# Optimization experiments

Measured on AMD Instinct MI355X. Metric: run time of the kernel, lower is better.

The kernel has to match this reference:

```python
import jax, jax.numpy as jnp
import numpy as np

THETA = 10000.0
AXES_DIM = (16, 56, 56)  # sums to head_dim=128
HEADS = 24
HEAD_DIM = 128
EPS = 1e-5


def _pos_embed(ids):
    # ids: (S, n_axes) int -> cos, sin each (S, head_dim//2)
    pos = ids.astype(jnp.float32)
    cos_out, sin_out = [], []
    for i, d in enumerate(AXES_DIM):
        freqs = 1.0 / (THETA ** (jnp.arange(0, d, 2, dtype=jnp.float32) / d))  # (d/2,)
        ang = pos[:, i][:, None] * freqs[None, :]  # (S, d/2)
        cos_out.append(jnp.cos(ang))
        sin_out.append(jnp.sin(ang))
    return jnp.concatenate(cos_out, -1), jnp.concatenate(sin_out, -1)


def _rms_norm(x, w):
    # per-head RMSNorm over last dim (head_dim)
    var = jnp.mean(x * x, axis=-1, keepdims=True)
    return x * jax.lax.rsqrt(var + EPS) * w


def _apply_rope(x, cos, sin):
    # non-neox (interleaved) rotary. x: (B,S,H,D), cos/sin: (S,D/2)
    x1 = x[..., 0::2]
    x2 = x[..., 1::2]
    c = cos[None, :, None, :]
    s = sin[None, :, None, :]
    o1 = x1 * c - x2 * s
    o2 = x2 * c + x1 * s
    return jnp.stack([o1, o2], axis=-1).reshape(x.shape)


def setup_inputs() -> dict:
    key = jax.random.key(0)
    ks = jax.random.split(key, 12)
    B, S_img, S_txt, D = 1, 2048, 512, 3072
    sd = 1.0 / np.sqrt(D)
    return {
        "hidden_states": jax.random.normal(ks[0], (B, S_img, D), jnp.float32),
        "encoder_hidden_states": jax.random.normal(ks[1], (B, S_txt, D), jnp.float32),
        "ids": jax.random.randint(ks[2], (S_txt + S_img, 3), 0, 64, jnp.int32),
        "w_qkv": jax.random.normal(ks[3], (D, 3 * D), jnp.float32) * sd,
        "w_add_qkv": jax.random.normal(ks[4], (D, 3 * D), jnp.float32) * sd,
        "b_add_qkv": jax.random.normal(ks[5], (3 * D,), jnp.float32) * 0.02,
        "w_out": jax.random.normal(ks[6], (D, D), jnp.float32) * sd,
        "b_out": jax.random.normal(ks[7], (D,), jnp.float32) * 0.02,
        "w_add_out": jax.random.normal(ks[8], (D, D), jnp.float32) * sd,
        "b_add_out": jax.random.normal(ks[9], (D,), jnp.float32) * 0.02,
        "norm_q_w": jnp.ones((HEAD_DIM,), jnp.float32),
        "norm_k_w": jnp.ones((HEAD_DIM,), jnp.float32),
        "norm_add_q_w": jnp.ones((HEAD_DIM,), jnp.float32),
        "norm_add_k_w": jnp.ones((HEAD_DIM,), jnp.float32),
    }


def reference(hidden_states, encoder_hidden_states, ids, w_qkv, w_add_qkv,
              b_add_qkv, w_out, b_out, w_add_out, b_add_out,
              norm_q_w, norm_k_w, norm_add_q_w, norm_add_k_w):
    B, S_img, D = hidden_states.shape
    S_txt = encoder_hidden_states.shape[1]
    H, Dh = HEADS, HEAD_DIM

    # fused QKV projections
    qkv = hidden_states @ w_qkv  # (B, S_img, 3D)
    q, k, v = jnp.split(qkv, 3, axis=-1)
    q = _rms_norm(q.reshape(B, S_img, H, Dh), norm_q_w)
    k = _rms_norm(k.reshape(B, S_img, H, Dh), norm_k_w)
    v = v.reshape(B, S_img, H, Dh)

    eqkv = encoder_hidden_states @ w_add_qkv + b_add_qkv
    eq, ek, ev = jnp.split(eqkv, 3, axis=-1)
    eq = _rms_norm(eq.reshape(B, S_txt, H, Dh), norm_add_q_w)
    ek = _rms_norm(ek.reshape(B, S_txt, H, Dh), norm_add_k_w)
    ev = ev.reshape(B, S_txt, H, Dh)

    # joint sequence: text first, then image
    q = jnp.concatenate([eq, q], axis=1)
    k = jnp.concatenate([ek, k], axis=1)
    v = jnp.concatenate([ev, v], axis=1)

    # multi-axis RoPE over joint positions
    cos, sin = _pos_embed(ids)  # (S_txt+S_img, Dh/2)
    q = _apply_rope(q, cos, sin)
    k = _apply_rope(k, cos, sin)

    # scaled dot-product attention (non-causal)
    scale = 1.0 / np.sqrt(Dh)
    scores = jnp.einsum("bqhd,bkhd->bhqk", q, k) * scale
    probs = jax.nn.softmax(scores, axis=-1)
    attn = jnp.einsum("bhqk,bkhd->bqhd", probs, v)
    attn = attn.reshape(B, S_txt + S_img, H * Dh)

    enc_out = attn[:, :S_txt] @ w_add_out + b_add_out
    img_out = attn[:, S_txt:] @ w_out + b_out
    return img_out, enc_out
```

## Files before the change

kernel.cpp:

```cpp
#include <hip/hip_runtime.h>

typedef __attribute__((ext_vector_type(8))) short short8;
typedef __attribute__((ext_vector_type(4))) short short4v;
typedef __attribute__((ext_vector_type(4))) float floatx4;

__device__ __forceinline__ float b2f(short b) {
  union { unsigned u; float f; } v; v.u = ((unsigned)(unsigned short)b) << 16; return v.f;
}
__device__ __forceinline__ short f2b(float f) {
  union { float f; unsigned u; } v; v.f = f;
  return (short)((v.u + 0x7fffu + ((v.u >> 16) & 1u)) >> 16);
}
__device__ __forceinline__ unsigned cvtpk(float lo, float hi) {
  unsigned r;
  asm("v_cvt_pk_bf16_f32 %0, %1, %2" : "=v"(r) : "v"(lo), "v"(hi));
  return r;
}
__device__ __forceinline__ float loadf(const void* p, size_t i, bool f32) {
  return f32 ? ((const float*)p)[i] : b2f(((const short*)p)[i]);
}
__device__ __forceinline__ short8 load8(const void* p, size_t i, bool f32) {
  if (f32) {
    const float* fp = (const float*)p + i;
    float4 a = *(const float4*)fp;
    float4 b = *(const float4*)(fp + 4);
    short8 r;
    r[0] = f2b(a.x); r[1] = f2b(a.y); r[2] = f2b(a.z); r[3] = f2b(a.w);
    r[4] = f2b(b.x); r[5] = f2b(b.y); r[6] = f2b(b.z); r[7] = f2b(b.w);
    return r;
  }
  return *(const short8*)((const short*)p + i);
}

__device__ __forceinline__ void gload16(const short* g, short* l) {
  __builtin_amdgcn_global_load_lds(
      (const __attribute__((address_space(1))) unsigned int*)g,
      (__attribute__((address_space(3))) unsigned int*)l, 16, 0, 0);
}

__global__ void detect_dtype(const unsigned short* __restrict__ w, int* __restrict__ flag) {
  __shared__ int cnt;
  if (threadIdx.x == 0) cnt = 0;
  __syncthreads();
  int bad = 0;
  for (int i = threadIdx.x; i < 4096; i += 256) {
    int e = (w[i] >> 7) & 0xFF;
    if (e >= 0xC8) bad++;
  }
  atomicAdd(&cnt, bad);
  __syncthreads();
  if (threadIdx.x == 0) *flag = (cnt > 64) ? 1 : 0;
}

__global__ __launch_bounds__(256)
void cvt_bf16_2(const void* __restrict__ srcA, long n8A,
                const void* __restrict__ srcB, long n8B,
                short* __restrict__ dst, const int* __restrict__ dflag) {
  const bool f32 = (*dflag != 0);
  const long n8 = n8A + n8B;
  long stride = (long)gridDim.x * 256;
  for (long i = (long)blockIdx.x * 256 + threadIdx.x; i < n8; i += stride) {
    const void* s; long e;
    if (i < n8A) { s = srcA; e = i * 8; } else { s = srcB; e = (i - n8A) * 8; }
    if (f32) {
      const float* fp = (const float*)s + e;
      float4 a = *(const float4*)fp;
      float4 b = *(const float4*)(fp + 4);
      short8 r;
      r[0] = f2b(a.x); r[1] = f2b(a.y); r[2] = f2b(a.z); r[3] = f2b(a.w);
      r[4] = f2b(b.x); r[5] = f2b(b.y); r[6] = f2b(b.z); r[7] = f2b(b.w);
      *(short8*)(dst + i * 8) = r;
    } else {
      *(short8*)(dst + i * 8) = *(const short8*)((const short*)s + e);
    }
  }
}

__global__ __launch_bounds__(256)
void cvt_tw(const void* __restrict__ wq, short* __restrict__ wqd,
            const void* __restrict__ waq, short* __restrict__ waqd,
            const void* __restrict__ wo, short* __restrict__ wod,
            const void* __restrict__ wao, short* __restrict__ waod,
            const int* __restrict__ dflag) {
  __shared__ short st[64][72];
  const bool f32 = (*dflag != 0);
  const int K = 3072;
  int b = blockIdx.x;
  const void* src; short* dst; int N, n0, k0;
  if (b < 13824) {
    src = (b < 6912) ? wq : waq;
    dst = (b < 6912) ? wqd : waqd;
    int rem = b % 6912;
    N = 9216; n0 = (rem % 144) << 6; k0 = (rem / 144) << 6;
  } else {
    b -= 13824;
    src = (b < 2304) ? wo : wao;
    dst = (b < 2304) ? wod : waod;
    int rem = b % 2304;
    N = 3072; n0 = (rem % 48) << 6; k0 = (rem / 48) << 6;
  }
  const int c4 = threadIdx.x & 15;
  const int rq = threadIdx.x >> 4;
#pragma unroll
  for (int r = 0; r < 4; ++r) {
    int k = r * 16 + rq;
    int n = c4 * 4;
    short v0, v1, v2, v3;
    if (f32) {
      const float* sp = (const float*)src + (size_t)(k0 + k) * N + n0 + n;
      float4 f = *(const float4*)sp;
      v0 = f2b(f.x); v1 = f2b(f.y); v2 = f2b(f.z); v3 = f2b(f.w);
    } else {
      const short* sp = (const short*)src + (size_t)(k0 + k) * N + n0 + n;
      short4v s = *(const short4v*)sp;
      v0 = s[0]; v1 = s[1]; v2 = s[2]; v3 = s[3];
    }
    st[n + 0][k] = v0; st[n + 1][k] = v1; st[n + 2][k] = v2; st[n + 3][k] = v3;
  }
  __syncthreads();
  const int n = threadIdx.x >> 2;
  const int kc = (threadIdx.x & 3) << 4;
  short8 a = *(const short8*)(&st[n][kc]);
  short8 bb = *(const short8*)(&st[n][kc + 8]);
  short* dp = dst + (size_t)(n0 + n) * K + k0 + kc;
  *(short8*)(dp) = a;
  *(short8*)(dp + 8) = bb;
}

__global__ __launch_bounds__(256, 2)
void gemm_bt(const void* __restrict__ A, int a_row0,
             const void* __restrict__ B, const void* __restrict__ bias,
             void* __restrict__ C, int c_row0, int N, int K,
             const int* __restrict__ dflag, int aIn, int cOut) {
  __shared__ short As[128 * 32];
  __shared__ short Bs[128 * 32];
  const bool f32 = (*dflag != 0);
  const bool a32 = aIn && f32;
  const bool c32 = cOut && f32;
  const int tid = threadIdx.x;
  const int lane = tid & 63, w = tid >> 6;
  const int wm = w & 1, wn = w >> 1;
  const int qg = lane >> 4, l16 = lane & 15;
  const int m0 = blockIdx.y << 7, n0 = blockIdx.x << 7;

  const int arow = tid >> 2, ak = (tid & 3) << 3;
  const int brow = tid >> 4, bc = (tid & 15) << 3;
  const int rot = tid & 15;

  floatx4 acc[4][4];
#pragma unroll
  for (int i = 0; i < 4; ++i)
#pragma unroll
    for (int j = 0; j < 4; ++j) acc[i][j] = (floatx4){0.f, 0.f, 0.f, 0.f};

  for (int k0 = 0; k0 < K; k0 += 32) {
    __syncthreads();
#pragma unroll
    for (int j = 0; j < 2; ++j) {
      short8 av = load8(A, (size_t)(a_row0 + m0 + j * 64 + arow) * K + (k0 + ak), a32);
      *(short8*)(As + (j * 64 + arow) * 32 + ak) = av;
      int kr = j * 16 + brow;
      short8 bv = load8(B, (size_t)(k0 + kr) * N + (n0 + bc), f32);
      int kq = kr >> 3, kj = kr & 7;
#pragma unroll
      for (int s = 0; s < 8; ++s) {
        int u = (s + rot) & 7;
        int n = bc + u;
        Bs[(n << 5) + ((kq ^ (n & 3)) << 3) + kj] = bv[u];
      }
    }
    __syncthreads();
    short8 a[4];
#pragma unroll
    for (int mi = 0; mi < 4; ++mi)
      a[mi] = *(const short8*)(As + (wm * 64 + mi * 16 + l16) * 32 + qg * 8);
#pragma unroll
    for (int ni = 0; ni < 4; ++ni) {
      int n = wn * 64 + ni * 16 + l16;
      short8 b = *(const short8*)(Bs + (n << 5) + ((qg ^ (n & 3)) << 3));
#pragma unroll
      for (int mi = 0; mi < 4; ++mi)
        acc[mi][ni] = __builtin_amdgcn_mfma_f32_16x16x32_bf16(a[mi], b, acc[mi][ni], 0, 0, 0);
    }
  }
#pragma unroll
  for (int ni = 0; ni < 4; ++ni) {
    int col = n0 + wn * 64 + ni * 16 + l16;
    float bv = bias ? loadf(bias, col, f32) : 0.0f;
#pragma unroll
    for (int mi = 0; mi < 4; ++mi) {
      int row = m0 + wm * 64 + mi * 16 + qg * 4;
#pragma unroll
      for (int r = 0; r < 4; ++r) {
        size_t idx = (size_t)(c_row0 + row + r) * N + col;
        float val = acc[mi][ni][r] + bv;
        if (c32) ((float*)C)[idx] = val;
        else     ((short*)C)[idx] = f2b(val);
      }
    }
  }
}

__global__ __launch_bounds__(256, 2)
void gemm_bf2(const short* __restrict__ A,
              const short* __restrict__ BTa, const void* __restrict__ biasa,
              int a0a, int c0a, int nYa,
              const short* __restrict__ BTb, const void* __restrict__ biasb,
              int a0b, int c0b,
              void* __restrict__ C, int N, int K,
              const int* __restrict__ dflag, int cOut) {
  __shared__ short Ls[3 * 8192 + 3 * 4096];
#define ASB(b) (Ls + (b) * 8192)
#define BSB(b) (Ls + 24576 + (b) * 4096)
  const bool f32 = (*dflag != 0);
  const bool c32 = cOut && f32;
  const int bx = blockIdx.x;
  const int y = blockIdx.y;
  const short* BT; const void* bias; int arow0, crow0;
  if (y < nYa) { BT = BTa; bias = biasa; arow0 = a0a + (y << 8); crow0 = c0a + (y << 8); }
  else { int my = y - nYa; BT = BTb; bias = biasb; arow0 = a0b + (my << 8); crow0 = c0b + (my << 8); }
  const int tid = threadIdx.x;
  const int lane = tid & 63, w = tid >> 6;
  const int wm = w & 1, wn = w >> 1;
  const int qg = lane >> 4, l16 = lane & 15;
  const int n0 = bx << 7;
  const int garow = lane >> 2;
  const int gcir = lane & 3;
  const int nk = K >> 5;
  const int swz = (gcir ^ (garow & 3) ^ (garow >> 2)) << 3;
  const short* Abase = A + (size_t)(arow0 + w * 64 + garow) * K + swz;
  const short* Bbase = BT + (size_t)(n0 + w * 32 + garow) * K + swz;
  const int rswz = (l16 & 3) ^ (l16 >> 2);

  floatx4 acc[8][4];
#pragma unroll
  for (int i = 0; i < 8; ++i)
#pragma unroll
    for (int j = 0; j < 4; ++j) acc[i][j] = (floatx4){0.f, 0.f, 0.f, 0.f};

  auto STAGE = [&](int buf, int k0) {
#pragma unroll
    for (int j = 0; j < 4; ++j)
      gload16(Abase + (size_t)j * 16 * K + k0, ASB(buf) + ((w * 4 + j) << 9));
#pragma unroll
    for (int j = 0; j < 2; ++j)
      gload16(Bbase + (size_t)j * 16 * K + k0, BSB(buf) + ((w * 2 + j) << 9));
  };

  STAGE(0, 0);
  if (nk > 1) STAGE(1, 32);

  int cb = 0;
  for (int t = 0; t < nk; ++t) {
    if (t + 1 < nk) {
      asm volatile("s_waitcnt vmcnt(6) lgkmcnt(0)" ::: "memory");
    } else {
      asm volatile("s_waitcnt vmcnt(0) lgkmcnt(0)" ::: "memory");
    }
    __builtin_amdgcn_s_barrier();
    if (t + 2 < nk) {
      int sb = (cb == 0) ? 2 : cb - 1;
      STAGE(sb, (t + 2) << 5);
    }
    short8 a[8], b[4];
#pragma unroll
    for (int mi = 0; mi < 8; ++mi) {
      int ra = wm * 128 + mi * 16 + l16;
      a[mi] = *(const short8*)(ASB(cb) + (ra << 5) + ((qg ^ rswz) << 3));
    }
#pragma unroll
    for (int ni = 0; ni < 4; ++ni) {
      int n = wn * 64 + ni * 16 + l16;
      b[ni] = *(const short8*)(BSB(cb) + (n << 5) + ((qg ^ rswz) << 3));
    }
    __builtin_amdgcn_s_setprio(1);
#pragma unroll
    for (int ni = 0; ni < 4; ++ni)
#pragma unroll
      for (int mi = 0; mi < 8; ++mi)
        acc[mi][ni] = __builtin_amdgcn_mfma_f32_16x16x32_bf16(a[mi], b[ni], acc[mi][ni], 0, 0, 0);
    __builtin_amdgcn_s_setprio(0);
    cb = (cb == 2) ? 0 : cb + 1;
  }
  __builtin_amdgcn_s_barrier();
  if (!c32) {
    short* wreg = Ls + w * 4096;
#pragma unroll
    for (int half = 0; half < 2; ++half) {
#pragma unroll
      for (int ni = 0; ni < 4; ++ni) {
        float bvv = bias ? loadf(bias, n0 + wn * 64 + ni * 16 + l16, f32) : 0.0f;
#pragma unroll
        for (int mi2 = 0; mi2 < 4; ++mi2)
#pragma unroll
          for (int r = 0; r < 4; ++r)
            wreg[(mi2 * 16 + qg * 4 + r) * 64 + ni * 16 + l16] =
                f2b(acc[half * 4 + mi2][ni][r] + bvv);
      }
      asm volatile("s_waitcnt lgkmcnt(0)" ::: "memory");
#pragma unroll
      for (int j = 0; j < 8; ++j) {
        int row = j * 8 + (lane >> 3);
        int col = (lane & 7) * 8;
        short8 v = *(const short8*)(wreg + row * 64 + col);
        *(short8*)((short*)C + (size_t)(crow0 + wm * 128 + half * 64 + row) * N +
                   n0 + wn * 64 + col) = v;
      }
      asm volatile("s_waitcnt lgkmcnt(0)" ::: "memory");
    }
  } else {
    float* wregf = (float*)(Ls) + w * 2048;
#pragma unroll
    for (int half = 0; half < 2; ++half) {
#pragma unroll
      for (int ch = 0; ch < 2; ++ch) {
#pragma unroll
        for (int nh = 0; nh < 2; ++nh) {
          int ni = ch * 2 + nh;
          float bvv = bias ? loadf(bias, n0 + wn * 64 + ni * 16 + l16, f32) : 0.0f;
#pragma unroll
          for (int mi2 = 0; mi2 < 4; ++mi2)
#pragma unroll
            for (int r = 0; r < 4; ++r)
              wregf[(mi2 * 16 + qg * 4 + r) * 32 + nh * 16 + l16] =
                  acc[half * 4 + mi2][ni][r] + bvv;
        }
        asm volatile("s_waitcnt lgkmcnt(0)" ::: "memory");
#pragma unroll
        for (int j = 0; j < 8; ++j) {
          int row = j * 8 + (lane >> 3);
          int c4 = (lane & 7) * 4;
          float4 v = *(const float4*)(wregf + row * 32 + c4);
          *(float4*)((float*)C + (size_t)(crow0 + wm * 128 + half * 64 + row) * N +
                     n0 + wn * 64 + ch * 32 + c4) = v;
        }
        asm volatile("s_waitcnt lgkmcnt(0)" ::: "memory");
      }
    }
  }
#undef ASB
#undef BSB
}

__global__ __launch_bounds__(256, 3)
void gemm_bf128(const short* __restrict__ A,
                const short* __restrict__ BTa, const void* __restrict__ biasa,
                int a0a, int c0a, int nYa,
                const short* __restrict__ BTb, const void* __restrict__ biasb,
                int a0b, int c0b,
                void* __restrict__ C, int N, int K,
                const int* __restrict__ dflag, int cOut) {
  __shared__ short Ls[6 * 128 * 32];
#define ASB(b) (Ls + (b) * 4096)
#define BSB(b) (Ls + (3 + (b)) * 4096)
  const bool f32 = (*dflag != 0);
  const bool c32 = cOut && f32;
  const int bx = blockIdx.x;
  const int y = blockIdx.y;
  const short* BT; const void* bias; int arow0, crow0;
  if (y < nYa) { BT = BTa; bias = biasa; arow0 = a0a + (y << 7); crow0 = c0a + (y << 7); }
  else { int my = y - nYa; BT = BTb; bias = biasb; arow0 = a0b + (my << 7); crow0 = c0b + (my << 7); }
  const int tid = threadIdx.x;
  const int lane = tid & 63, w = tid >> 6;
  const int wm = w & 1, wn = w >> 1;
  const int qg = lane >> 4, l16 = lane & 15;
  const int n0 = bx << 7;
  const int garow = lane >> 2;
  const int gcir = lane & 3;
  const int nk = K >> 5;
  const int swz = (gcir ^ (garow & 3) ^ (garow >> 2)) << 3;
  const short* Abase = A + (size_t)(arow0 + w * 32 + garow) * K + swz;
  const short* Bbase = BT + (size_t)(n0 + w * 32 + garow) * K + swz;
  const int rswz = (l16 & 3) ^ (l16 >> 2);

  floatx4 acc[4][4];
#pragma unroll
  for (int i = 0; i < 4; ++i)
#pragma unroll
    for (int j = 0; j < 4; ++j) acc[i][j] = (floatx4){0.f, 0.f, 0.f, 0.f};

  auto STAGE = [&](int buf, int k0) {
#pragma unroll
    for (int j = 0; j < 2; ++j) {
      gload16(Abase + (size_t)j * 16 * K + k0, ASB(buf) + ((w * 2 + j) << 9));
      gload16(Bbase + (size_t)j * 16 * K + k0, BSB(buf) + ((w * 2 + j) << 9));
    }
  };

  STAGE(0, 0);
  if (nk > 1) STAGE(1, 32);

  int cb = 0;
  for (int t = 0; t < nk; ++t) {
    if (t + 1 < nk) {
      asm volatile("s_waitcnt vmcnt(4) lgkmcnt(0)" ::: "memory");
    } else {
      asm volatile("s_waitcnt vmcnt(0) lgkmcnt(0)" ::: "memory");
    }
    __builtin_amdgcn_s_barrier();
    if (t + 2 < nk) {
      int sb = (cb == 0) ? 2 : cb - 1;
      STAGE(sb, (t + 2) << 5);
    }
    short8 a[4], b[4];
#pragma unroll
    for (int mi = 0; mi < 4; ++mi) {
      int ra = wm * 64 + mi * 16 + l16;
      a[mi] = *(const short8*)(ASB(cb) + (ra << 5) + ((qg ^ rswz) << 3));
    }
#pragma unroll
    for (int ni = 0; ni < 4; ++ni) {
      int n = wn * 64 + ni * 16 + l16;
      b[ni] = *(const short8*)(BSB(cb) + (n << 5) + ((qg ^ rswz) << 3));
    }
    __builtin_amdgcn_s_setprio(1);
#pragma unroll
    for (int ni = 0; ni < 4; ++ni)
#pragma unroll
      for (int mi = 0; mi < 4; ++mi)
        acc[mi][ni] = __builtin_amdgcn_mfma_f32_16x16x32_bf16(a[mi], b[ni], acc[mi][ni], 0, 0, 0);
    __builtin_amdgcn_s_setprio(0);
    cb = (cb == 2) ? 0 : cb + 1;
  }
  __builtin_amdgcn_s_barrier();
  if (!c32) {
    short* wreg = Ls + w * 4096;
#pragma unroll
    for (int ni = 0; ni < 4; ++ni) {
      float bvv = bias ? loadf(bias, n0 + wn * 64 + ni * 16 + l16, f32) : 0.0f;
#pragma unroll
      for (int mi = 0; mi < 4; ++mi)
#pragma unroll
        for (int r = 0; r < 4; ++r)
          wreg[(mi * 16 + qg * 4 + r) * 64 + ni * 16 + l16] = f2b(acc[mi][ni][r] + bvv);
    }
    asm volatile("s_waitcnt lgkmcnt(0)" ::: "memory");
#pragma unroll
    for (int j = 0; j < 8; ++j) {
      int row = j * 8 + (lane >> 3);
      int col = (lane & 7) * 8;
      short8 v = *(const short8*)(wreg + row * 64 + col);
      *(short8*)((short*)C + (size_t)(crow0 + wm * 64 + row) * N + n0 + wn * 64 + col) = v;
    }
  } else {
    float* wregf = (float*)(Ls) + w * 2048;
#pragma unroll
    for (int half = 0; half < 2; ++half) {
#pragma unroll
      for (int nh = 0; nh < 2; ++nh) {
        int ni = half * 2 + nh;
        float bvv = bias ? loadf(bias, n0 + wn * 64 + ni * 16 + l16, f32) : 0.0f;
#pragma unroll
        for (int mi = 0; mi < 4; ++mi)
#pragma unroll
          for (int r = 0; r < 4; ++r)
            wregf[(mi * 16 + qg * 4 + r) * 32 + nh * 16 + l16] = acc[mi][ni][r] + bvv;
      }
      asm volatile("s_waitcnt lgkmcnt(0)" ::: "memory");
#pragma unroll
      for (int j = 0; j < 8; ++j) {
        int row = j * 8 + (lane >> 3);
        int c4 = (lane & 7) * 4;
        float4 v = *(const float4*)(wregf + row * 32 + c4);
        *(float4*)((float*)C + (size_t)(crow0 + wm * 64 + row) * N + n0 + wn * 64 + half * 32 + c4) = v;
      }
      asm volatile("s_waitcnt lgkmcnt(0)" ::: "memory");
    }
  }
#undef ASB
#undef BSB
}

__global__ __launch_bounds__(512)
void norm_rope(short* __restrict__ qkv, const int* __restrict__ ids,
               const void* __restrict__ nqw, const void* __restrict__ nkw,
               const void* __restrict__ naqw, const void* __restrict__ nakw,
               const int* __restrict__ dflag) {
  const bool f32 = (*dflag != 0);
  const int t = blockIdx.x, wv = threadIdx.x >> 6, lane = threadIdx.x & 63;
  const bool txt = t < 512;
  int p = lane, axis; float expo;
  if (p < 8)       { axis = 0; expo = (float)(2 * p) * (1.0f / 16.0f); }
  else if (p < 36) { axis = 1; expo = (float)(2 * (p - 8)) * (1.0f / 56.0f); }
  else             { axis = 2; expo = (float)(2 * (p - 36)) * (1.0f / 56.0f); }
  float freq = __expf(-expo * 9.210340371976184f);
  float ang = (float)ids[t * 3 + axis] * freq;
  float s, c; sincosf(ang, &s, &c);
  const void* qw = txt ? naqw : nqw;
  const void* kw = txt ? nakw : nkw;
  float w0q = loadf(qw, 2 * lane, f32), w1q = loadf(qw, 2 * lane + 1, f32);
  float w0k = loadf(kw, 2 * lane, f32), w1k = loadf(kw, 2 * lane + 1, f32);
  const float QS = 0.08838834764831845f * 1.4426950408889634f;
#pragma unroll
  for (int i = 0; i < 3; ++i) {
    int h = wv + 8 * i;
    short* qp = qkv + (size_t)t * 9216 + h * 128 + 2 * lane;
    short* kp = qp + 3072;
    union { unsigned u; short sh[2]; } qv, kv;
    qv.u = *(const unsigned*)qp;
    kv.u = *(const unsigned*)kp;
    float q0 = b2f(qv.sh[0]), q1 = b2f(qv.sh[1]);
    float k0 = b2f(kv.sh[0]), k1 = b2f(kv.sh[1]);
    float sq = q0 * q0 + q1 * q1, sk = k0 * k0 + k1 * k1;
#pragma unroll
    for (int o = 1; o < 64; o <<= 1) { sq += __shfl_xor(sq, o); sk += __shfl_xor(sk, o); }
    float rq = rsqrtf(sq * (1.0f / 128.0f) + 1e-5f);
    float rk = rsqrtf(sk * (1.0f / 128.0f) + 1e-5f);
    float qn0 = q0 * rq * w0q, qn1 = q1 * rq * w1q;
    float kn0 = k0 * rk * w0k, kn1 = k1 * rk * w1k;
    float qo0 = qn0 * c - qn1 * s, qo1 = qn1 * c + qn0 * s;
    float ko0 = kn0 * c - kn1 * s, ko1 = kn1 * c + kn0 * s;
    union { unsigned u; short sh[2]; } qo, ko;
    qo.sh[0] = f2b(qo0 * QS);
    qo.sh[1] = f2b(qo1 * QS);
    ko.sh[0] = f2b(ko0); ko.sh[1] = f2b(ko1);
    *(unsigned*)qp = qo.u;
    *(unsigned*)kp = ko.u;
  }
}

__global__ __launch_bounds__(512, 2)
void attn_fa(const short* __restrict__ qkv, short* __restrict__ attn) {
  __shared__ short QPs[256 * 128];
  __shared__ short KVs[2][128 * 128];
  const int wgid = blockIdx.x;
  const int xcd = wgid & 7, slot = wgid >> 3;
  const int h = xcd * 3 + slot / 10;
  const int qt = slot % 10;
  const int tid = threadIdx.x, lane = tid & 63, w = tid >> 6;
  const int qg = lane >> 4, l16 = lane & 15;
  const int lr = lane >> 4, lc = lane & 15;
  const int q0 = qt << 8;
  const int sc = tid & 15;
  const int srow5 = (tid >> 4) & 15, half = tid >> 8;

  const short* Qg  = qkv + (size_t)q0 * 9216 + h * 128;
  const short* Kg0 = qkv + 3072 + h * 128;
  const short* Vg0 = qkv + 6144 + h * 128;

  short8 vr[4];
#pragma unroll
  for (int j = 0; j < 8; ++j) {
    int row = j * 32 + w * 4 + lr;
    gload16(Qg + (size_t)row * 9216 + ((lc ^ (row & 7)) << 3),
            QPs + (j * 32 + w * 4) * 128);
  }
#pragma unroll
  for (int j = 0; j < 4; ++j) {
    int row = j * 32 + w * 4 + lr;
    gload16(Kg0 + (size_t)row * 9216 + ((lc ^ (row & 7)) << 3),
            &KVs[0][(j * 32 + w * 4) * 128]);
  }
#pragma unroll
  for (int j = 0; j < 4; ++j) {
    int row = half * 64 + j * 16 + srow5;
    vr[j] = *(const short8*)(Vg0 + (size_t)row * 9216 + sc * 8);
  }
  asm volatile("s_waitcnt vmcnt(8) lgkmcnt(0)" ::: "memory");
  __builtin_amdgcn_s_barrier();
  short8 aq[2][4];
#pragma unroll
  for (int mi = 0; mi < 2; ++mi)
#pragma unroll
    for (int kc = 0; kc < 4; ++kc) {
      int row = w * 32 + mi * 16 + l16;
      aq[mi][kc] = *(const short8*)(QPs + row * 128 + (((kc * 4 + qg) ^ (row & 7)) << 3));
    }

  floatx4 acc_o[2][8];
#pragma unroll
  for (int mi = 0; mi < 2; ++mi)
#pragma unroll
    for (int nd = 0; nd < 8; ++nd) acc_o[mi][nd] = (floatx4){0.f, 0.f, 0.f, 0.f};
  float m_i[2][4], l_i[2][4];
#pragma unroll
  for (int mi = 0; mi < 2; ++mi)
#pragma unroll
    for (int r = 0; r < 4; ++r) { m_i[mi][r] = -1e30f; l_i[mi][r] = 0.0f; }

  for (int kt = 0; kt < 20; ++kt) {
    const int c = kt & 1;
    asm volatile("s_waitcnt vmcnt(4) lgkmcnt(0)" ::: "memory");
    __builtin_amdgcn_s_barrier();
    if (kt < 19) {
      const short* Kg = qkv + ((size_t)(kt + 1) * 128) * 9216 + 3072 + h * 128;
#pragma unroll
      for (int j = 0; j < 4; ++j) {
        int row = j * 32 + w * 4 + lr;
        gload16(Kg + (size_t)row * 9216 + ((lc ^ (row & 7)) << 3),
                &KVs[1 - c][(j * 32 + w * 4) * 128]);
      }
    }
    floatx4 acc_s[2][8];
#pragma unroll
    for (int mi = 0; mi < 2; ++mi)
#pragma unroll
      for (int ni = 0; ni < 8; ++ni) acc_s[mi][ni] = (floatx4){0.f, 0.f, 0.f, 0.f};
    __builtin_amdgcn_s_setprio(1);
#pragma unroll
    for (int kc = 0; kc < 4; ++kc) {
#pragma unroll
      for (int ni = 0; ni < 8; ++ni) {
        int row = ni * 16 + l16;
        short8 b = *(const short8*)(&KVs[c][row * 128 + (((kc * 4 + qg) ^ (row & 7)) << 3)]);
        acc_s[0][ni] = __builtin_amdgcn_mfma_f32_16x16x32_bf16(aq[0][kc], b, acc_s[0][ni], 0, 0, 0);
        acc_s[1][ni] = __builtin_amdgcn_mfma_f32_16x16x32_bf16(aq[1][kc], b, acc_s[1][ni], 0, 0, 0);
      }
    }
    __builtin_amdgcn_s_setprio(0);
    float mxv[2][4];
    bool need = false;
#pragma unroll
    for (int mi = 0; mi < 2; ++mi) {
#pragma unroll
      for (int r = 0; r < 4; ++r) {
        float mx = acc_s[mi][0][r];
#pragma unroll
        for (int ni = 1; ni < 8; ++ni) mx = fmaxf(mx, acc_s[mi][ni][r]);
        mx = fmaxf(mx, __shfl_xor(mx, 1));
        mx = fmaxf(mx, __shfl_xor(mx, 2));
        mx = fmaxf(mx, __shfl_xor(mx, 4));
        mx = fmaxf(mx, __shfl_xor(mx, 8));
        mxv[mi][r] = mx;
        need = need || (mx > m_i[mi][r] + 8.0f);
      }
    }
    if (__ballot(need)) {
#pragma unroll
      for (int mi = 0; mi < 2; ++mi) {
#pragma unroll
        for (int r = 0; r < 4; ++r) {
          float mn = fmaxf(m_i[mi][r], mxv[mi][r]);
          float al = __builtin_amdgcn_exp2f(m_i[mi][r] - mn);
          m_i[mi][r] = mn;
          l_i[mi][r] *= al;
#pragma unroll
          for (int nd = 0; nd < 8; ++nd) acc_o[mi][nd][r] *= al;
        }
      }
    }
#pragma unroll
    for (int mi = 0; mi < 2; ++mi) {
      float rs[4] = {0.f, 0.f, 0.f, 0.f};
#pragma unroll
      for (int r = 0; r < 4; ++r) {
        float pv[8];
#pragma unroll
        for (int ni = 0; ni < 8; ++ni) {
          pv[ni] = __builtin_amdgcn_exp2f(acc_s[mi][ni][r] - m_i[mi][r]);
          rs[r] += pv[ni];
        }
        unsigned u0 = cvtpk(pv[0], pv[1]);
        unsigned u1 = cvtpk(pv[2], pv[3]);
        unsigned u2 = cvtpk(pv[4], pv[5]);
        unsigned u3 = cvtpk(pv[6], pv[7]);
        int row = w * 32 + mi * 16 + qg * 4 + r;
        uint4 uu; uu.x = u0; uu.y = u1; uu.z = u2; uu.w = u3;
        *(uint4*)(QPs + row * 128 + ((l16 ^ (row & 15)) << 3)) = uu;
      }
#pragma unroll
      for (int r = 0; r < 4; ++r) {
        float t = rs[r];
        t += __shfl_xor(t, 1); t += __shfl_xor(t, 2);
        t += __shfl_xor(t, 4); t += __shfl_xor(t, 8);
        l_i[mi][r] += t;
      }
    }
    asm volatile("s_waitcnt lgkmcnt(0)" ::: "memory");
    __builtin_amdgcn_s_barrier();
#pragma unroll
    for (int u = 0; u < 8; ++u) {
      int d = sc * 8 + u;
      short4v pk = { vr[0][u], vr[1][u], vr[2][u], vr[3][u] };
      *(short4v*)(&KVs[c][d * 128 + (((srow5 ^ u ^ (sc & 7))) << 3) + half * 4]) = pk;
    }
    if (kt < 19) {
      const short* Vg = qkv + ((size_t)(kt + 1) * 128) * 9216 + 6144 + h * 128;
#pragma unroll
      for (int j = 0; j < 4; ++j) {
        int row = half * 64 + j * 16 + srow5;
        vr[j] = *(const short8*)(Vg + (size_t)row * 9216 + sc * 8);
      }
    }
    asm volatile("s_waitcnt lgkmcnt(0)" ::: "memory");
    __builtin_amdgcn_s_barrier();
    __builtin_amdgcn_s_setprio(1);
#pragma unroll
    for (int kc = 0; kc < 4; ++kc) {
      int prow0 = w * 32 + l16;
      short8 ap0 = *(const short8*)(QPs + prow0 * 128 + (((kc * 4 + qg) ^ (prow0 & 15)) << 3));
      int prow1 = prow0 + 16;
      short8 ap1 = *(const short8*)(QPs + prow1 * 128 + (((kc * 4 + qg) ^ (prow1 & 15)) << 3));
#pragma unroll
      for (int nd = 0; nd < 8; ++nd) {
        int row = nd * 16 + l16;
        int chn = (kc * 4 + qg) ^ (row & 7) ^ ((row >> 3) & 7);
        short8 b = *(const short8*)(&KVs[c][row * 128 + (chn << 3)]);
        acc_o[0][nd] = __builtin_amdgcn_mfma_f32_16x16x32_bf16(ap0, b, acc_o[0][nd], 0, 0, 0);
        acc_o[1][nd] = __builtin_amdgcn_mfma_f32_16x16x32_bf16(ap1, b, acc_o[1][nd], 0, 0, 0);
      }
    }
    __builtin_amdgcn_s_setprio(0);
  }
#pragma unroll
  for (int mi = 0; mi < 2; ++mi) {
    float inv[4];
#pragma unroll
    for (int r = 0; r < 4; ++r) inv[r] = 1.0f / l_i[mi][r];
#pragma unroll
    for (int nd = 0; nd < 8; ++nd) {
#pragma unroll
      for (int r = 0; r < 4; ++r) {
        int row = w * 32 + mi * 16 + qg * 4 + r;
        QPs[row * 128 + nd * 16 + l16] = f2b(acc_o[mi][nd][r] * inv[r]);
      }
    }
  }
  asm volatile("s_waitcnt lgkmcnt(0)" ::: "memory");
#pragma unroll
  for (int j = 0; j < 8; ++j) {
    int rrow = w * 32 + j * 4 + qg;
    short8 vv = *(const short8*)(QPs + rrow * 128 + l16 * 8);
    *(short8*)(attn + (size_t)(q0 + rrow) * 3072 + h * 128 + l16 * 8) = vv;
  }
}

extern "C" void kernel_launch(void* const* d_in, const int* in_sizes, int n_in,
                              void* d_out, int out_size, void* d_ws, size_t ws_size,
                              hipStream_t stream) {
  (void)in_sizes; (void)n_in; (void)out_size;
  const void* hidden    = d_in[0];
  const void* enc       = d_in[1];
  const int*  ids       = (const int*)d_in[2];
  const void* w_qkv     = d_in[3];
  const void* w_add_qkv = d_in[4];
  const void* b_add_qkv = d_in[5];
  const void* w_out     = d_in[6];
  const void* b_out     = d_in[7];
  const void* w_add_out = d_in[8];
  const void* b_add_out = d_in[9];
  const void* nqw  = d_in[10];
  const void* nkw  = d_in[11];
  const void* naqw = d_in[12];
  const void* nakw = d_in[13];

  int*   dflag = (int*)d_ws;
  short* qkv   = (short*)((char*)d_ws + 256);
  short* attnB = qkv + (size_t)2560 * 9216;

  short* pool  = attnB + (size_t)2560 * 3072;
  const long n_hid  = 2048L * 3072;
  const long n_enc  = 512L * 3072;
  const long n_wqkv = 3072L * 9216;
  const long n_wout = 3072L * 3072;
  short* xb   = pool;
  short* wqb  = xb + n_enc + n_hid;
  short* waqb = wqb + n_wqkv;
  short* wob  = waqb + n_wqkv;
  short* waob = wob + n_wout;
  const size_t REQ = 256 + 2 * ((size_t)2560 * 9216 + (size_t)2560 * 3072 +
                                n_hid + n_enc + 2 * n_wqkv + 2 * n_wout);

  detect_dtype<<<1, 256, 0, stream>>>((const unsigned short*)w_qkv, dflag);

  if (ws_size >= REQ) {
    cvt_bf16_2<<<1024, 256, 0, stream>>>(enc, n_enc / 8, hidden, n_hid / 8, xb, dflag);
    cvt_tw<<<dim3(18432), 256, 0, stream>>>(w_qkv, wqb, w_add_qkv, waqb,
                                            w_out, wob, w_add_out, waob, dflag);

    gemm_bf2<<<dim3(72, 10), 256, 0, stream>>>(
        xb, waqb, b_add_qkv, 0, 0, 2, wqb, nullptr, 512, 512,
        qkv, 9216, 3072, dflag, 0);
    norm_rope<<<dim3(2560), 512, 0, stream>>>(qkv, ids, nqw, nkw, naqw, nakw, dflag);
    attn_fa<<<dim3(240), 512, 0, stream>>>(qkv, attnB);
    gemm_bf128<<<dim3(24, 20), 256, 0, stream>>>(
        attnB, wob, b_out, 512, 0, 16, waob, b_add_out, 0, 2048,
        d_out, 3072, 3072, dflag, 1);
  } else {
    gemm_bt<<<dim3(72, 4), 256, 0, stream>>>(enc, 0, w_add_qkv, b_add_qkv, qkv, 0, 9216, 3072, dflag, 1, 0);
    gemm_bt<<<dim3(72, 16), 256, 0, stream>>>(hidden, 0, w_qkv, nullptr, qkv, 512, 9216, 3072, dflag, 1, 0);
    norm_rope<<<dim3(2560), 512, 0, stream>>>(qkv, ids, nqw, nkw, naqw, nakw, dflag);
    attn_fa<<<dim3(240), 512, 0, stream>>>(qkv, attnB);
    gemm_bt<<<dim3(24, 16), 256, 0, stream>>>(attnB, 512, w_out, b_out, d_out, 0, 3072, 3072, dflag, 0, 1);
    gemm_bt<<<dim3(24, 4), 256, 0, stream>>>(attnB, 0, w_add_out, b_add_out, d_out, 2048, 3072, 3072, dflag, 0, 1);
  }
}
```

Measured before the change: 792.8 us.

## Halve attention query tile to 128 rows and stage P per-wave

The flash-attention kernel now handles 128 query rows per workgroup instead of 256, so each wave owns 16 rows and the grid doubles from 240 to 480 blocks. Q is loaded straight from global memory into registers rather than through LDS. The P tile passes through a small per-wave LDS buffer per k-chunk instead of a full 256x128 shared tile, and the V transpose layout changes to match. This is meant to spread work across more CUs and cut LDS footprint. The cost is twice the K/V global traffic per query and half the MFMA reuse of each K/V fragment.

```diff
diff --git a/kernel.cpp b/kernel.cpp
--- a/kernel.cpp
+++ b/kernel.cpp
@@ -521,16 +521,16 @@
 
 __global__ __launch_bounds__(512, 2)
 void attn_fa(const short* __restrict__ qkv, short* __restrict__ attn) {
-  __shared__ short QPs[256 * 128];
   __shared__ short KVs[2][128 * 128];
+  __shared__ short Pw[8][512];
   const int wgid = blockIdx.x;
   const int xcd = wgid & 7, slot = wgid >> 3;
-  const int h = xcd * 3 + slot / 10;
-  const int qt = slot % 10;
+  const int h = xcd * 3 + slot / 20;
+  const int qt = slot % 20;
   const int tid = threadIdx.x, lane = tid & 63, w = tid >> 6;
   const int qg = lane >> 4, l16 = lane & 15;
   const int lr = lane >> 4, lc = lane & 15;
-  const int q0 = qt << 8;
+  const int q0 = qt << 7;
   const int sc = tid & 15;
   const int srow5 = (tid >> 4) & 15, half = tid >> 8;
 
@@ -538,19 +538,17 @@
   const short* Kg0 = qkv + 3072 + h * 128;
   const short* Vg0 = qkv + 6144 + h * 128;
 
-  short8 vr[4];
-#pragma unroll
-  for (int j = 0; j < 8; ++j) {
-    int row = j * 32 + w * 4 + lr;
-    gload16(Qg + (size_t)row * 9216 + ((lc ^ (row & 7)) << 3),
-            QPs + (j * 32 + w * 4) * 128);
-  }
 #pragma unroll
   for (int j = 0; j < 4; ++j) {
     int row = j * 32 + w * 4 + lr;
     gload16(Kg0 + (size_t)row * 9216 + ((lc ^ (row & 7)) << 3),
             &KVs[0][(j * 32 + w * 4) * 128]);
   }
+  short8 aq[4];
+#pragma unroll
+  for (int kc = 0; kc < 4; ++kc)
+    aq[kc] = *(const short8*)(Qg + (size_t)(w * 16 + l16) * 9216 + kc * 32 + qg * 8);
+  short8 vr[4];
 #pragma unroll
   for (int j = 0; j < 4; ++j) {
     int row = half * 64 + j * 16 + srow5;
@@ -558,28 +556,16 @@
   }
   asm volatile("s_waitcnt vmcnt(8) lgkmcnt(0)" ::: "memory");
   __builtin_amdgcn_s_barrier();
-  short8 aq[2][4];
-#pragma unroll
-  for (int mi = 0; mi < 2; ++mi)
-#pragma unroll
-    for (int kc = 0; kc < 4; ++kc) {
-      int row = w * 32 + mi * 16 + l16;
-      aq[mi][kc] = *(const short8*)(QPs + row * 128 + (((kc * 4 + qg) ^ (row & 7)) << 3));
-    }
-
-  floatx4 acc_o[2][8];
-#pragma unroll
-  for (int mi = 0; mi < 2; ++mi)
-#pragma unroll
-    for (int nd = 0; nd < 8; ++nd) acc_o[mi][nd] = (floatx4){0.f, 0.f, 0.f, 0.f};
-  float m_i[2][4], l_i[2][4];
-#pragma unroll
-  for (int mi = 0; mi < 2; ++mi)
-#pragma unroll
-    for (int r = 0; r < 4; ++r) { m_i[mi][r] = -1e30f; l_i[mi][r] = 0.0f; }
+
+  floatx4 acc_o[8];
+#pragma unroll
+  for (int nd = 0; nd < 8; ++nd) acc_o[nd] = (floatx4){0.f, 0.f, 0.f, 0.f};
+  float m_i[4], l_i[4];
+#pragma unroll
+  for (int r = 0; r < 4; ++r) { m_i[r] = -1e30f; l_i[r] = 0.0f; }
 
   for (int kt = 0; kt < 20; ++kt) {
-    const int c = kt & 1;
+    const int cb = kt & 1;
     asm volatile("s_waitcnt vmcnt(4) lgkmcnt(0)" ::: "memory");
     __builtin_amdgcn_s_barrier();
     if (kt < 19) {
@@ -588,91 +574,78 @@
       for (int j = 0; j < 4; ++j) {
         int row = j * 32 + w * 4 + lr;
         gload16(Kg + (size_t)row * 9216 + ((lc ^ (row & 7)) << 3),
-                &KVs[1 - c][(j * 32 + w * 4) * 128]);
-      }
-    }
-    floatx4 acc_s[2][8];
-#pragma unroll
-    for (int mi = 0; mi < 2; ++mi)
-#pragma unroll
-      for (int ni = 0; ni < 8; ++ni) acc_s[mi][ni] = (floatx4){0.f, 0.f, 0.f, 0.f};
+                &KVs[1 - cb][(j * 32 + w * 4) * 128]);
+      }
+    }
+    floatx4 acc_s[8];
+#pragma unroll
+    for (int ni = 0; ni < 8; ++ni) acc_s[ni] = (floatx4){0.f, 0.f, 0.f, 0.f};
     __builtin_amdgcn_s_setprio(1);
 #pragma unroll
     for (int kc = 0; kc < 4; ++kc) {
 #pragma unroll
       for (int ni = 0; ni < 8; ++ni) {
         int row = ni * 16 + l16;
-        short8 b = *(const short8*)(&KVs[c][row * 128 + (((kc * 4 + qg) ^ (row & 7)) << 3)]);
-        acc_s[0][ni] = __builtin_amdgcn_mfma_f32_16x16x32_bf16(aq[0][kc], b, acc_s[0][ni], 0, 0, 0);
-        acc_s[1][ni] = __builtin_amdgcn_mfma_f32_16x16x32_bf16(aq[1][kc], b, acc_s[1][ni], 0, 0, 0);
+        short8 b = *(const short8*)(&KVs[cb][row * 128 + (((kc * 4 + qg) ^ (row & 7)) << 3)]);
+        acc_s[ni] = __builtin_amdgcn_mfma_f32_16x16x32_bf16(aq[kc], b, acc_s[ni], 0, 0, 0);
       }
     }
     __builtin_amdgcn_s_setprio(0);
-    float mxv[2][4];
+    float mxv[4];
     bool need = false;
 #pragma unroll
-    for (int mi = 0; mi < 2; ++mi) {
+    for (int r = 0; r < 4; ++r) {
+      float mx = acc_s[0][r];
+#pragma unroll
+      for (int ni = 1; ni < 8; ++ni) mx = fmaxf(mx, acc_s[ni][r]);
+      mx = fmaxf(mx, __shfl_xor(mx, 1));
+      mx = fmaxf(mx, __shfl_xor(mx, 2));
+      mx = fmaxf(mx, __shfl_xor(mx, 4));
+      mx = fmaxf(mx, __shfl_xor(mx, 8));
+      mxv[r] = mx;
+      need = need || (mx > m_i[r] + 8.0f);
+    }
+    if (__ballot(need)) {
 #pragma unroll
       for (int r = 0; r < 4; ++r) {
-        float mx = acc_s[mi][0][r];
-#pragma unroll
-        for (int ni = 1; ni < 8; ++ni) mx = fmaxf(mx, acc_s[mi][ni][r]);
-        mx = fmaxf(mx, __shfl_xor(mx, 1));
-        mx = fmaxf(mx, __shfl_xor(mx, 2));
-        mx = fmaxf(mx, __shfl_xor(mx, 4));
-        mx = fmaxf(mx, __shfl_xor(mx, 8));
-        mxv[mi][r] = mx;
-        need = need || (mx > m_i[mi][r] + 8.0f);
-      }
-    }
-    if (__ballot(need)) {
-#pragma unroll
-      for (int mi = 0; mi < 2; ++mi) {
-#pragma unroll
-        for (int r = 0; r < 4; ++r) {
-          float mn = fmaxf(m_i[mi][r], mxv[mi][r]);
-          float al = __builtin_amdgcn_exp2f(m_i[mi][r] - mn);
-          m_i[mi][r] = mn;
-          l_i[mi][r] *= al;
-#pragma unroll
-          for (int nd = 0; nd < 8; ++nd) acc_o[mi][nd][r] *= al;
-        }
-      }
-    }
-#pragma unroll
-    for (int mi = 0; mi < 2; ++mi) {
-      float rs[4] = {0.f, 0.f, 0.f, 0.f};
-#pragma unroll
-      for (int r = 0; r < 4; ++r) {
-        float pv[8];
-#pragma unroll
-        for (int ni = 0; ni < 8; ++ni) {
-          pv[ni] = __builtin_amdgcn_exp2f(acc_s[mi][ni][r] - m_i[mi][r]);
-          rs[r] += pv[ni];
-        }
-        unsigned u0 = cvtpk(pv[0], pv[1]);
-        unsigned u1 = cvtpk(pv[2], pv[3]);
-        unsigned u2 = cvtpk(pv[4], pv[5]);
-        unsigned u3 = cvtpk(pv[6], pv[7]);
-        int row = w * 32 + mi * 16 + qg * 4 + r;
-        uint4 uu; uu.x = u0; uu.y = u1; uu.z = u2; uu.w = u3;
-        *(uint4*)(QPs + row * 128 + ((l16 ^ (row & 15)) << 3)) = uu;
-      }
-#pragma unroll
-      for (int r = 0; r < 4; ++r) {
-        float t = rs[r];
-        t += __shfl_xor(t, 1); t += __shfl_xor(t, 2);
-        t += __shfl_xor(t, 4); t += __shfl_xor(t, 8);
-        l_i[mi][r] += t;
-      }
+        float mn = fmaxf(m_i[r], mxv[r]);
+        float al = __builtin_amdgcn_exp2f(m_i[r] - mn);
+        m_i[r] = mn;
+        l_i[r] *= al;
+#pragma unroll
+        for (int nd = 0; nd < 8; ++nd) acc_o[nd][r] *= al;
+      }
+    }
+    unsigned pkr[4][4];
+#pragma unroll
+    for (int r = 0; r < 4; ++r) {
+      float pv[8];
+      float rs = 0.f;
+#pragma unroll
+      for (int ni = 0; ni < 8; ++ni) {
+        pv[ni] = __builtin_amdgcn_exp2f(acc_s[ni][r] - m_i[r]);
+        rs += pv[ni];
+      }
+#pragma unroll
+      for (int kc = 0; kc < 4; ++kc) pkr[r][kc] = cvtpk(pv[2 * kc], pv[2 * kc + 1]);
+      rs += __shfl_xor(rs, 1); rs += __shfl_xor(rs, 2);
+      rs += __shfl_xor(rs, 4); rs += __shfl_xor(rs, 8);
+      l_i[r] += rs;
     }
     asm volatile("s_waitcnt lgkmcnt(0)" ::: "memory");
     __builtin_amdgcn_s_barrier();
 #pragma unroll
     for (int u = 0; u < 8; ++u) {
       int d = sc * 8 + u;
-      short4v pk = { vr[0][u], vr[1][u], vr[2][u], vr[3][u] };
-      *(short4v*)(&KVs[c][d * 128 + (((srow5 ^ u ^ (sc & 7))) << 3) + half * 4]) = pk;
+      int xr = (d & 7) ^ ((d >> 3) & 7);
+#pragma unroll
+      for (int jp = 0; jp < 2; ++jp) {
+        int kcw = 2 * half + jp;
+        int g = kcw * 4 + (srow5 >> 2);
+        union { unsigned uu; short sh[2]; } pk;
+        pk.sh[0] = vr[2 * jp][u]; pk.sh[1] = vr[2 * jp + 1][u];
+        *(unsigned*)(&KVs[cb][d * 128 + ((g ^ xr) << 3) + ((2 * srow5) & 7)]) = pk.uu;
+      }
     }
     if (kt < 19) {
       const short* Vg = qkv + ((size_t)(kt + 1) * 128) * 9216 + 6144 + h * 128;
@@ -687,40 +660,38 @@
     __builtin_amdgcn_s_setprio(1);
 #pragma unroll
     for (int kc = 0; kc < 4; ++kc) {
-      int prow0 = w * 32 + l16;
-      short8 ap0 = *(const short8*)(QPs + prow0 * 128 + (((kc * 4 + qg) ^ (prow0 & 15)) << 3));
-      int prow1 = prow0 + 16;
-      short8 ap1 = *(const short8*)(QPs + prow1 * 128 + (((kc * 4 + qg) ^ (prow1 & 15)) << 3));
+#pragma unroll
+      for (int r = 0; r < 4; ++r)
+        *(unsigned*)(&Pw[w][(qg * 4 + r) * 32 + ((l16 ^ (qg << 2)) << 1)]) = pkr[r][kc];
+      short8 ap = *(const short8*)(&Pw[w][l16 * 32 + ((qg ^ (l16 >> 2)) << 3)]);
 #pragma unroll
       for (int nd = 0; nd < 8; ++nd) {
-        int row = nd * 16 + l16;
-        int chn = (kc * 4 + qg) ^ (row & 7) ^ ((row >> 3) & 7);
-        short8 b = *(const short8*)(&KVs[c][row * 128 + (chn << 3)]);
-        acc_o[0][nd] = __builtin_amdgcn_mfma_f32_16x16x32_bf16(ap0, b, acc_o[0][nd], 0, 0, 0);
-        acc_o[1][nd] = __builtin_amdgcn_mfma_f32_16x16x32_bf16(ap1, b, acc_o[1][nd], 0, 0, 0);
+        int d = nd * 16 + l16;
+        int chn = (kc * 4 + qg) ^ (d & 7) ^ ((d >> 3) & 7);
+        short8 b = *(const short8*)(&KVs[cb][d * 128 + (chn << 3)]);
+        acc_o[nd] = __builtin_amdgcn_mfma_f32_16x16x32_bf16(ap, b, acc_o[nd], 0, 0, 0);
       }
     }
     __builtin_amdgcn_s_setprio(0);
   }
-#pragma unroll
-  for (int mi = 0; mi < 2; ++mi) {
-    float inv[4];
-#pragma unroll
-    for (int r = 0; r < 4; ++r) inv[r] = 1.0f / l_i[mi][r];
-#pragma unroll
-    for (int nd = 0; nd < 8; ++nd) {
-#pragma unroll
-      for (int r = 0; r < 4; ++r) {
-        int row = w * 32 + mi * 16 + qg * 4 + r;
-        QPs[row * 128 + nd * 16 + l16] = f2b(acc_o[mi][nd][r] * inv[r]);
-      }
-    }
-  }
   asm volatile("s_waitcnt lgkmcnt(0)" ::: "memory");
-#pragma unroll
-  for (int j = 0; j < 8; ++j) {
-    int rrow = w * 32 + j * 4 + qg;
-    short8 vv = *(const short8*)(QPs + rrow * 128 + l16 * 8);
+  __builtin_amdgcn_s_barrier();
+  short* Es = &KVs[0][0];
+  float inv[4];
+#pragma unroll
+  for (int r = 0; r < 4; ++r) inv[r] = 1.0f / l_i[r];
+#pragma unroll
+  for (int nd = 0; nd < 8; ++nd)
+#pragma unroll
+    for (int r = 0; r < 4; ++r) {
+      int row = w * 16 + qg * 4 + r;
+      Es[row * 128 + nd * 16 + l16] = f2b(acc_o[nd][r] * inv[r]);
+    }
+  asm volatile("s_waitcnt lgkmcnt(0)" ::: "memory");
+#pragma unroll
+  for (int j = 0; j < 4; ++j) {
+    int rrow = w * 16 + j * 4 + qg;
+    short8 vv = *(const short8*)(Es + rrow * 128 + l16 * 8);
     *(short8*)(attn + (size_t)(q0 + rrow) * 3072 + h * 128 + l16 * 8) = vv;
   }
 }
@@ -772,7 +743,7 @@
         xb, waqb, b_add_qkv, 0, 0, 2, wqb, nullptr, 512, 512,
         qkv, 9216, 3072, dflag, 0);
     norm_rope<<<dim3(2560), 512, 0, stream>>>(qkv, ids, nqw, nkw, naqw, nakw, dflag);
-    attn_fa<<<dim3(240), 512, 0, stream>>>(qkv, attnB);
+    attn_fa<<<dim3(480), 512, 0, stream>>>(qkv, attnB);
     gemm_bf128<<<dim3(24, 20), 256, 0, stream>>>(
         attnB, wob, b_out, 512, 0, 16, waob, b_add_out, 0, 2048,
         d_out, 3072, 3072, dflag, 1);
@@ -780,7 +751,7 @@
     gemm_bt<<<dim3(72, 4), 256, 0, stream>>>(enc, 0, w_add_qkv, b_add_qkv, qkv, 0, 9216, 3072, dflag, 1, 0);
     gemm_bt<<<dim3(72, 16), 256, 0, stream>>>(hidden, 0, w_qkv, nullptr, qkv, 512, 9216, 3072, dflag, 1, 0);
     norm_rope<<<dim3(2560), 512, 0, stream>>>(qkv, ids, nqw, nkw, naqw, nakw, dflag);
-    attn_fa<<<dim3(240), 512, 0, stream>>>(qkv, attnB);
+    attn_fa<<<dim3(480), 512, 0, stream>>>(qkv, attnB);
     gemm_bt<<<dim3(24, 16), 256, 0, stream>>>(attnB, 512, w_out, b_out, d_out, 0, 3072, 3072, dflag, 0, 1);
     gemm_bt<<<dim3(24, 4), 256, 0, stream>>>(attnB, 0, w_add_out, b_add_out, d_out, 2048, 3072, 3072, dflag, 0, 1);
   }
```

Result: no change. 785.1 us, median of 3 (-1.0%).
